# Kernel optimization log

Measured on AMD Instinct MI355X. Metric: run time of the kernel, lower is better.

The kernel has to match this reference:

```python
import jax, jax.numpy as jnp
import numpy as np

N, E, D = 100000, 1600000, 64
L = 3          # num_layers
EPS = 1e-5     # LayerNorm eps


def setup_inputs() -> dict:
    key = jax.random.key(0)
    ks = jax.random.split(key, 8)
    s = 0.05
    return {
        "x": jax.random.normal(ks[0], (N, D), jnp.float32),
        "edge_src": jax.random.randint(ks[1], (E,), 0, N, jnp.int32),
        "edge_dst": jax.random.randint(ks[2], (E,), 0, N, jnp.int32),
        # SAGEConv: lin_l (on aggregated neighbors, with bias), lin_r (root, no bias)
        "w_l": (jax.random.normal(ks[3], (L, D, D)) * s).astype(jnp.float32),
        "b_l": jnp.zeros((L, D), jnp.float32),
        "w_r": (jax.random.normal(ks[4], (L, D, D)) * s).astype(jnp.float32),
        # LayerNorm affine params per layer
        "gamma": jnp.ones((L, D), jnp.float32),
        "beta": jnp.zeros((L, D), jnp.float32),
        # residual projection (layer 0 only; Identity afterwards)
        "w_res": (jax.random.normal(ks[5], (D, D)) * s).astype(jnp.float32),
        "b_res": jnp.zeros((D,), jnp.float32),
        # final fc
        "w_fc": (jax.random.normal(ks[6], (D, D)) * s).astype(jnp.float32),
        "b_fc": jnp.zeros((D,), jnp.float32),
    }


def _layer_norm(h, g, b):
    mu = jnp.mean(h, axis=-1, keepdims=True)
    var = jnp.var(h, axis=-1, keepdims=True)
    return (h - mu) * jax.lax.rsqrt(var + EPS) * g + b


def reference(x, edge_src, edge_dst, w_l, b_l, w_r, gamma, beta, w_res, b_res, w_fc, b_fc):
    n = x.shape[0]
    # in-degree for mean aggregation (nodes with no in-edges get 0 aggregate)
    deg = jax.ops.segment_sum(jnp.ones(edge_dst.shape, x.dtype), edge_dst, num_segments=n)
    inv_deg = jnp.where(deg > 0, 1.0 / jnp.maximum(deg, 1.0), 0.0)[:, None]  # [N,1]
    for i in range(L):
        residual = x @ w_res + b_res if i == 0 else x
        # SAGEConv mean aggregation: gather source feats, scatter-sum at dst, divide by degree
        agg = jax.ops.segment_sum(x[edge_src], edge_dst, num_segments=n) * inv_deg  # [N,D]
        h = agg @ w_l[i] + b_l[i] + x @ w_r[i]
        h = jax.nn.relu(_layer_norm(h, gamma[i], beta[i]))
        # dropout is inactive in eval mode
        x = h + residual
    return x @ w_fc + b_fc
```

## Files before the change

### kernel.cpp

```cpp
#include <hip/hip_runtime.h>

typedef unsigned short u16;
typedef __bf16 bf16x8 __attribute__((ext_vector_type(8)));
typedef float f32x4 __attribute__((ext_vector_type(4)));

#define D 64
#define LPITCH 136
#define SPITCH 72
#define CHUNKS 512
#define BSHIFT 9

__device__ __forceinline__ float b2f(u16 u) {
    unsigned v = ((unsigned)u) << 16;
    float f;
    __builtin_memcpy(&f, &v, 4);
    return f;
}
__device__ __forceinline__ float u2f_lo(unsigned u) {
    unsigned v = u << 16;
    float f;
    __builtin_memcpy(&f, &v, 4);
    return f;
}
__device__ __forceinline__ float u2f_hi(unsigned u) {
    unsigned v = u & 0xFFFF0000u;
    float f;
    __builtin_memcpy(&f, &v, 4);
    return f;
}
__device__ __forceinline__ u16 f2b(float f) {
    unsigned u;
    __builtin_memcpy(&u, &f, 4);
    u = u + 0x7FFFu + ((u >> 16) & 1u);
    return (u16)(u >> 16);
}
__device__ __forceinline__ bf16x8 ld_frag(const u16* p) {
    union { uint4 u; bf16x8 b; } cv;
    cv.u = *(const uint4*)p;
    return cv.b;
}

__global__ __launch_bounds__(256) void binA_kernel(const int* __restrict__ dst, int E,
                                                   int* __restrict__ H,
                                                   int nbuck, int eper) {
    __shared__ int hist[256];
    int t = threadIdx.x;
    int c = blockIdx.x;
    hist[t] = 0;
    __syncthreads();
    int beg = c * eper;
    int end = min(beg + eper, E);
    for (int i = beg + t; i < end; i += 256) {
        atomicAdd(&hist[dst[i] >> BSHIFT], 1);
    }
    __syncthreads();
    if (t < nbuck) H[c * nbuck + t] = hist[t];
}

__global__ __launch_bounds__(256) void binS2_kernel(const int* __restrict__ H,
                                                    int* __restrict__ Orel,
                                                    int* __restrict__ T,
                                                    int nbuck) {
    __shared__ int ss[256];
    int b = blockIdx.x;
    int t = threadIdx.x;
    int h0 = H[(2 * t) * nbuck + b];
    int h1 = H[(2 * t + 1) * nbuck + b];
    ss[t] = h0 + h1;
    __syncthreads();
    for (int off = 1; off < 256; off <<= 1) {
        int v = (t >= off) ? ss[t - off] : 0;
        __syncthreads();
        ss[t] += v;
        __syncthreads();
    }
    int excl = ss[t] - h0 - h1;
    Orel[(2 * t) * nbuck + b] = excl;
    Orel[(2 * t + 1) * nbuck + b] = excl + h0;
    if (t == 255) T[b] = ss[255];
}

__global__ __launch_bounds__(256) void binT_kernel(const int* __restrict__ T, int nbuck,
                                                   int* __restrict__ base,
                                                   int* __restrict__ row_ptr, int N) {
    __shared__ int sm[256];
    int t = threadIdx.x;
    int v = (t < nbuck) ? T[t] : 0;
    sm[t] = v;
    __syncthreads();
    for (int off = 1; off < 256; off <<= 1) {
        int u = (t >= off) ? sm[t - off] : 0;
        __syncthreads();
        sm[t] += u;
        __syncthreads();
    }
    if (t < nbuck) base[t] = sm[t] - v;
    if (t == 255) {
        base[nbuck] = sm[255];
        row_ptr[N] = sm[255];
    }
}

__global__ __launch_bounds__(256) void binB_kernel(const int* __restrict__ src,
                                                   const int* __restrict__ dst, int E,
                                                   const int* __restrict__ base,
                                                   const int* __restrict__ Orel,
                                                   int* __restrict__ staging,
                                                   int nbuck, int eper) {
    __shared__ int pos[256];
    int t = threadIdx.x;
    int c = blockIdx.x;
    if (t < nbuck) pos[t] = base[t] + Orel[c * nbuck + t];
    __syncthreads();
    int beg = c * eper;
    int end = min(beg + eper, E);
    const int mask = (1 << BSHIFT) - 1;
    for (int i = beg + t; i < end; i += 256) {
        int d = dst[i];
        int b = d >> BSHIFT;
        int p = atomicAdd(&pos[b], 1);
        staging[p] = src[i] | ((d & mask) << 17);
    }
}

__global__ __launch_bounds__(256) void binC_kernel(const int* __restrict__ staging,
                                                   const int* __restrict__ base,
                                                   int* __restrict__ row_ptr,
                                                   float* __restrict__ inv_deg,
                                                   int* __restrict__ col, int N) {
    __shared__ int cnt[512];
    __shared__ int lrp[512];
    __shared__ int sm[256];
    int b = blockIdx.x;
    int t = threadIdx.x;
    int node0 = b << BSHIFT;
    int nn = min(1 << BSHIFT, N - node0);
    cnt[t] = 0;
    cnt[t + 256] = 0;
    __syncthreads();
    int sbeg = base[b], send = base[b + 1];
    for (int i = sbeg + t; i < send; i += 256) {
        atomicAdd(&cnt[staging[i] >> 17], 1);
    }
    __syncthreads();
    int c0 = cnt[2 * t], c1 = cnt[2 * t + 1];
    sm[t] = c0 + c1;
    __syncthreads();
    for (int off = 1; off < 256; off <<= 1) {
        int v = (t >= off) ? sm[t - off] : 0;
        __syncthreads();
        sm[t] += v;
        __syncthreads();
    }
    int excl = sm[t] - c0 - c1;
    lrp[2 * t] = excl;
    lrp[2 * t + 1] = excl + c0;
    __syncthreads();
    for (int i = t; i < nn; i += 256) {
        row_ptr[node0 + i] = sbeg + lrp[i];
        int dd = cnt[i];
        inv_deg[node0 + i] = dd > 0 ? 1.0f / (float)dd : 0.0f;
    }
    __syncthreads();
    for (int i = sbeg + t; i < send; i += 256) {
        int word = staging[i];
        int ld = word >> 17;
        int k = atomicSub(&cnt[ld], 1) - 1;
        col[sbeg + lrp[ld] + k] = word & 0x1FFFF;
    }
}

__global__ __launch_bounds__(256) void prep_w(const float* __restrict__ wl,
                                              const float* __restrict__ wr,
                                              const float* __restrict__ wres,
                                              const float* __restrict__ wfc,
                                              u16* __restrict__ WtL,
                                              u16* __restrict__ WresT,
                                              u16* __restrict__ WfcT) {
    int gid = blockIdx.x * 256 + threadIdx.x;
    int gstr = gridDim.x * 256;
    for (int idx = gid; idx < 3 * 64 * 128; idx += gstr) {
        int l = idx >> 13;
        int rem = idx & 8191;
        int n = rem >> 7;
        int k = rem & 127;
        float v = (k < 64) ? wl[l * 4096 + k * 64 + n] : wr[l * 4096 + (k - 64) * 64 + n];
        WtL[idx] = f2b(v);
    }
    for (int idx = gid; idx < 4096; idx += gstr) {
        int n = idx >> 6, k = idx & 63;
        WresT[idx] = f2b(wres[k * 64 + n]);
        WfcT[idx] = f2b(wfc[k * 64 + n]);
    }
}

__global__ __launch_bounds__(256) void cvt_kernel(const float* __restrict__ xf,
                                                  u16* __restrict__ xb, int total4) {
    int i = blockIdx.x * 256 + threadIdx.x;
    int stride = gridDim.x * 256;
    for (; i < total4; i += stride) {
        float4 v = *(const float4*)(xf + i * 4);
        ushort4 o;
        o.x = f2b(v.x); o.y = f2b(v.y); o.z = f2b(v.z); o.w = f2b(v.w);
        *(ushort4*)(xb + i * 4) = o;
    }
}

__global__ __launch_bounds__(256, 4) void layer_kernel(const u16* __restrict__ xb_in,
                                                       const int* __restrict__ row_ptr,
                                                       const int* __restrict__ col,
                                                       const float* __restrict__ inv_deg,
                                                       const u16* __restrict__ Wt,
                                                       const float* __restrict__ bl,
                                                       const float* __restrict__ gam,
                                                       const float* __restrict__ bet,
                                                       const u16* __restrict__ WresT,
                                                       const float* __restrict__ bres,
                                                       u16* __restrict__ xb_out,
                                                       int N, int layer0) {
    __shared__ __align__(16) u16 sA[64 * LPITCH];
    __shared__ __align__(16) u16 sB[64 * LPITCH];
    int tid = threadIdx.x;
    int base = blockIdx.x * 64;
    int lane = tid & 63;
    int w = tid >> 6;

#pragma unroll
    for (int i = 0; i < 4; i++) {
        int idx = i * 256 + tid;
        int r = idx >> 4, c = idx & 15;
        *(uint4*)&sB[r * LPITCH + c * 8] = *(const uint4*)(Wt + idx * 8);
    }
#pragma unroll
    for (int i = 0; i < 2; i++) {
        int idx = i * 256 + tid;
        int r = idx >> 3, c = idx & 7;
        int node = base + r;
        uint4 v = make_uint4(0, 0, 0, 0);
        if (node < N) v = *(const uint4*)(xb_in + node * D + c * 8);
        *(uint4*)&sA[r * LPITCH + 64 + c * 8] = v;
    }

    int slot = lane >> 3;
    int chunk = lane & 7;
#pragma unroll
    for (int r = 0; r < 2; r++) {
        int node_l = w * 16 + r * 8 + slot;
        int node = base + node_l;
        float a0 = 0, a1 = 0, a2 = 0, a3 = 0, a4 = 0, a5 = 0, a6 = 0, a7 = 0;
        uint4 o = make_uint4(0, 0, 0, 0);
        if (node < N) {
            int e = row_ptr[node], end = row_ptr[node + 1];
#define ACC(v)                                          \
    a0 += u2f_lo(v.x); a1 += u2f_hi(v.x);               \
    a2 += u2f_lo(v.y); a3 += u2f_hi(v.y);               \
    a4 += u2f_lo(v.z); a5 += u2f_hi(v.z);               \
    a6 += u2f_lo(v.w); a7 += u2f_hi(v.w);
            for (; e + 3 < end; e += 4) {
                int s0 = col[e], s1 = col[e + 1], s2 = col[e + 2], s3 = col[e + 3];
                uint4 v0 = *(const uint4*)(xb_in + s0 * D + chunk * 8);
                uint4 v1 = *(const uint4*)(xb_in + s1 * D + chunk * 8);
                uint4 v2 = *(const uint4*)(xb_in + s2 * D + chunk * 8);
                uint4 v3 = *(const uint4*)(xb_in + s3 * D + chunk * 8);
                ACC(v0) ACC(v1) ACC(v2) ACC(v3)
            }
            if (e + 1 < end) {
                int s0 = col[e], s1 = col[e + 1];
                uint4 v0 = *(const uint4*)(xb_in + s0 * D + chunk * 8);
                uint4 v1 = *(const uint4*)(xb_in + s1 * D + chunk * 8);
                ACC(v0) ACC(v1)
                e += 2;
            }
            if (e < end) {
                int s0 = col[e];
                uint4 v0 = *(const uint4*)(xb_in + s0 * D + chunk * 8);
                ACC(v0)
            }
#undef ACC
            float m = inv_deg[node];
            o.x = (unsigned)f2b(a0 * m) | ((unsigned)f2b(a1 * m) << 16);
            o.y = (unsigned)f2b(a2 * m) | ((unsigned)f2b(a3 * m) << 16);
            o.z = (unsigned)f2b(a4 * m) | ((unsigned)f2b(a5 * m) << 16);
            o.w = (unsigned)f2b(a6 * m) | ((unsigned)f2b(a7 * m) << 16);
        }
        *(uint4*)&sA[node_l * LPITCH + chunk * 8] = o;
    }
    __syncthreads();

    int q = lane >> 4;
    int ln = lane & 15;
    f32x4 acc[4] = {{0, 0, 0, 0}, {0, 0, 0, 0}, {0, 0, 0, 0}, {0, 0, 0, 0}};
    f32x4 accr[4] = {{0, 0, 0, 0}, {0, 0, 0, 0}, {0, 0, 0, 0}, {0, 0, 0, 0}};
    const u16* aRow = &sA[(w * 16 + ln) * LPITCH];

#pragma unroll
    for (int c = 0; c < 4; c++) {
        bf16x8 a = ld_frag(&aRow[c * 32 + q * 8]);
#pragma unroll
        for (int t = 0; t < 4; t++) {
            bf16x8 b = ld_frag(&sB[(t * 16 + ln) * LPITCH + c * 32 + q * 8]);
            acc[t] = __builtin_amdgcn_mfma_f32_16x16x32_bf16(a, b, acc[t], 0, 0, 0);
        }
    }
    if (layer0) {
#pragma unroll
        for (int c = 0; c < 2; c++) {
            bf16x8 a = ld_frag(&aRow[64 + c * 32 + q * 8]);
#pragma unroll
            for (int t = 0; t < 4; t++) {
                bf16x8 b = ld_frag(WresT + (t * 16 + ln) * 64 + c * 32 + q * 8);
                accr[t] = __builtin_amdgcn_mfma_f32_16x16x32_bf16(a, b, accr[t], 0, 0, 0);
            }
        }
    }

    float bcol[4], gcol[4], btcol[4], brcol[4];
#pragma unroll
    for (int t = 0; t < 4; t++) {
        int colI = t * 16 + ln;
        bcol[t] = bl[colI];
        gcol[t] = gam[colI];
        btcol[t] = bet[colI];
        brcol[t] = layer0 ? bres[colI] : 0.f;
    }
#pragma unroll
    for (int t = 0; t < 4; t++)
#pragma unroll
        for (int r = 0; r < 4; r++) acc[t][r] += bcol[t];

    float ps[4], pq[4];
#pragma unroll
    for (int r = 0; r < 4; r++) {
        float s = 0, s2 = 0;
#pragma unroll
        for (int t = 0; t < 4; t++) { float h = acc[t][r]; s += h; s2 += h * h; }
        ps[r] = s; pq[r] = s2;
    }
    for (int off = 1; off < 16; off <<= 1) {
#pragma unroll
        for (int r = 0; r < 4; r++) {
            ps[r] += __shfl_xor(ps[r], off, 64);
            pq[r] += __shfl_xor(pq[r], off, 64);
        }
    }
#pragma unroll
    for (int r = 0; r < 4; r++) {
        int nb = w * 16 + q * 4 + r;
        int node = base + nb;
        if (node >= N) continue;
        float mu = ps[r] * (1.f / 64.f);
        float var = pq[r] * (1.f / 64.f) - mu * mu;
        var = var < 0.f ? 0.f : var;
        float rstd = rsqrtf(var + 1e-5f);
#pragma unroll
        for (int t = 0; t < 4; t++) {
            int colI = t * 16 + ln;
            float hn = (acc[t][r] - mu) * rstd * gcol[t] + btcol[t];
            hn = hn > 0.f ? hn : 0.f;
            float res = layer0 ? (accr[t][r] + brcol[t])
                               : b2f(sA[nb * LPITCH + 64 + colI]);
            xb_out[node * D + colI] = f2b(hn + res);
        }
    }
}

__global__ __launch_bounds__(256) void fc_kernel(const u16* __restrict__ xbin,
                                                 const u16* __restrict__ WfcT,
                                                 const float* __restrict__ bfc,
                                                 float* __restrict__ out, int N) {
    __shared__ __align__(16) u16 sA[64 * SPITCH];
    __shared__ __align__(16) u16 sB[64 * SPITCH];
    int tid = threadIdx.x;
    int base = blockIdx.x * 64;
#pragma unroll
    for (int i = 0; i < 2; i++) {
        int idx = i * 256 + tid;
        int r = idx >> 3, c = idx & 7;
        int node = base + r;
        uint4 v = make_uint4(0, 0, 0, 0);
        if (node < N) v = *(const uint4*)(xbin + node * D + c * 8);
        *(uint4*)&sA[r * SPITCH + c * 8] = v;
        *(uint4*)&sB[r * SPITCH + c * 8] = *(const uint4*)(WfcT + idx * 8);
    }
    __syncthreads();
    int lane = tid & 63;
    int w = tid >> 6, q = lane >> 4, ln = lane & 15;
    f32x4 acc[4] = {{0, 0, 0, 0}, {0, 0, 0, 0}, {0, 0, 0, 0}, {0, 0, 0, 0}};
#pragma unroll
    for (int c = 0; c < 2; c++) {
        bf16x8 a = ld_frag(&sA[(w * 16 + ln) * SPITCH + c * 32 + q * 8]);
#pragma unroll
        for (int t = 0; t < 4; t++) {
            bf16x8 b = ld_frag(&sB[(t * 16 + ln) * SPITCH + c * 32 + q * 8]);
            acc[t] = __builtin_amdgcn_mfma_f32_16x16x32_bf16(a, b, acc[t], 0, 0, 0);
        }
    }
#pragma unroll
    for (int r = 0; r < 4; r++) {
        int node = base + w * 16 + q * 4 + r;
        if (node >= N) continue;
#pragma unroll
        for (int t = 0; t < 4; t++) {
            int colI = t * 16 + ln;
            out[node * D + colI] = acc[t][r] + bfc[colI];
        }
    }
}

extern "C" void kernel_launch(void* const* d_in, const int* in_sizes, int n_in,
                              void* d_out, int out_size, void* d_ws, size_t ws_size,
                              hipStream_t stream) {
    const float* x_in = (const float*)d_in[0];
    const int* e_src = (const int*)d_in[1];
    const int* e_dst = (const int*)d_in[2];
    const float* w_l = (const float*)d_in[3];
    const float* b_l = (const float*)d_in[4];
    const float* w_r = (const float*)d_in[5];
    const float* gam = (const float*)d_in[6];
    const float* bet = (const float*)d_in[7];
    const float* w_res = (const float*)d_in[8];
    const float* b_res = (const float*)d_in[9];
    const float* w_fc = (const float*)d_in[10];
    const float* b_fc = (const float*)d_in[11];
    float* out = (float*)d_out;

    const int N = in_sizes[0] / D;
    const int E = in_sizes[1];
    const int nbuck = ((N - 1) >> BSHIFT) + 1;
    const int eper = (E + CHUNKS - 1) / CHUNKS;

    size_t o = 0;
    auto carve = [&](size_t bytes) {
        size_t cur = o;
        o += (bytes + 255) & ~(size_t)255;
        return (char*)d_ws + cur;
    };
    int* row_ptr = (int*)carve((size_t)(N + 1) * 4);
    float* inv_deg = (float*)carve((size_t)N * 4);
    int* colA = (int*)carve((size_t)E * 4);
    int* staging = (int*)carve((size_t)E * 4);
    int* Hh = (int*)carve((size_t)CHUNKS * nbuck * 4);
    int* Orel = (int*)carve((size_t)CHUNKS * nbuck * 4);
    int* Tb = (int*)carve((size_t)nbuck * 4);
    int* baseB = (int*)carve((size_t)(nbuck + 1) * 4);
    u16* WtL = (u16*)carve(3 * 64 * 128 * 2);
    u16* WresT = (u16*)carve(64 * 64 * 2);
    u16* WfcT = (u16*)carve(64 * 64 * 2);
    u16* xbA = (u16*)carve((size_t)N * D * 2);
    u16* xbB = (u16*)carve((size_t)N * D * 2);

    binA_kernel<<<CHUNKS, 256, 0, stream>>>(e_dst, E, Hh, nbuck, eper);
    binS2_kernel<<<nbuck, 256, 0, stream>>>(Hh, Orel, Tb, nbuck);
    binT_kernel<<<1, 256, 0, stream>>>(Tb, nbuck, baseB, row_ptr, N);
    binB_kernel<<<CHUNKS, 256, 0, stream>>>(e_src, e_dst, E, baseB, Orel, staging, nbuck, eper);
    binC_kernel<<<nbuck, 256, 0, stream>>>(staging, baseB, row_ptr, inv_deg, colA, N);

    prep_w<<<32, 256, 0, stream>>>(w_l, w_r, w_res, w_fc, WtL, WresT, WfcT);
    cvt_kernel<<<1024, 256, 0, stream>>>(x_in, xbA, N * D / 4);

    int gridT = (N + 63) / 64;

    layer_kernel<<<gridT, 256, 0, stream>>>(xbA, row_ptr, colA, inv_deg, WtL,
                                            b_l, gam, bet, WresT, b_res, xbB, N, 1);
    layer_kernel<<<gridT, 256, 0, stream>>>(xbB, row_ptr, colA, inv_deg, WtL + 8192,
                                            b_l + 64, gam + 64, bet + 64, WresT, b_res,
                                            xbA, N, 0);
    layer_kernel<<<gridT, 256, 0, stream>>>(xbA, row_ptr, colA, inv_deg, WtL + 16384,
                                            b_l + 128, gam + 128, bet + 128, WresT, b_res,
                                            xbB, N, 0);
    fc_kernel<<<gridT, 256, 0, stream>>>(xbB, WfcT, b_fc, out, N);
}
```

Measured before the change: 289.9 us.

## Fuse final FC into last layer, drop weight LDS staging, halve binning chunks

Folds the final fully-connected projection into the third layer kernel, which writes its bf16 result back into LDS and runs the FC MFMA in place. This removes one launch and a full round trip of the activations through global memory. Layer weights are now read as MFMA fragments straight from global/L2 instead of being staged into a second LDS buffer, which frees LDS so the occupancy hint can rise from 4 to 6 blocks. The binning histogram uses 256 chunks with a simpler one-entry-per-thread scan. The extra final_ branch and the global weight fragment loads may cost some latency in exchange.

Result: slower. 330.0 us (+13.8%).

```diff
diff --git a/kernel.cpp b/kernel.cpp
--- a/kernel.cpp
+++ b/kernel.cpp
@@ -7,7 +7,7 @@
 #define D 64
 #define LPITCH 136
 #define SPITCH 72
-#define CHUNKS 512
+#define CHUNKS 256
 #define BSHIFT 9
 
 __device__ __forceinline__ float b2f(u16 u) {
@@ -64,9 +64,8 @@
     __shared__ int ss[256];
     int b = blockIdx.x;
     int t = threadIdx.x;
-    int h0 = H[(2 * t) * nbuck + b];
-    int h1 = H[(2 * t + 1) * nbuck + b];
-    ss[t] = h0 + h1;
+    int h = H[t * nbuck + b];
+    ss[t] = h;
     __syncthreads();
     for (int off = 1; off < 256; off <<= 1) {
         int v = (t >= off) ? ss[t - off] : 0;
@@ -74,9 +73,7 @@
         ss[t] += v;
         __syncthreads();
     }
-    int excl = ss[t] - h0 - h1;
-    Orel[(2 * t) * nbuck + b] = excl;
-    Orel[(2 * t + 1) * nbuck + b] = excl + h0;
+    Orel[t * nbuck + b] = ss[t] - h;
     if (t == 255) T[b] = ss[255];
 }
 
@@ -206,7 +203,7 @@
     }
 }
 
-__global__ __launch_bounds__(256, 4) void layer_kernel(const u16* __restrict__ xb_in,
+__global__ __launch_bounds__(256, 6) void layer_kernel(const u16* __restrict__ xb_in,
                                                        const int* __restrict__ row_ptr,
                                                        const int* __restrict__ col,
                                                        const float* __restrict__ inv_deg,
@@ -216,21 +213,17 @@
                                                        const float* __restrict__ bet,
                                                        const u16* __restrict__ WresT,
                                                        const float* __restrict__ bres,
+                                                       const u16* __restrict__ WfcT,
+                                                       const float* __restrict__ bfc,
                                                        u16* __restrict__ xb_out,
-                                                       int N, int layer0) {
+                                                       float* __restrict__ fout,
+                                                       int N, int layer0, int final_) {
     __shared__ __align__(16) u16 sA[64 * LPITCH];
-    __shared__ __align__(16) u16 sB[64 * LPITCH];
     int tid = threadIdx.x;
     int base = blockIdx.x * 64;
     int lane = tid & 63;
     int w = tid >> 6;
 
-#pragma unroll
-    for (int i = 0; i < 4; i++) {
-        int idx = i * 256 + tid;
-        int r = idx >> 4, c = idx & 15;
-        *(uint4*)&sB[r * LPITCH + c * 8] = *(const uint4*)(Wt + idx * 8);
-    }
 #pragma unroll
     for (int i = 0; i < 2; i++) {
         int idx = i * 256 + tid;
@@ -298,7 +291,7 @@
         bf16x8 a = ld_frag(&aRow[c * 32 + q * 8]);
 #pragma unroll
         for (int t = 0; t < 4; t++) {
-            bf16x8 b = ld_frag(&sB[(t * 16 + ln) * LPITCH + c * 32 + q * 8]);
+            bf16x8 b = ld_frag(Wt + (t * 16 + ln) * 128 + c * 32 + q * 8);
             acc[t] = __builtin_amdgcn_mfma_f32_16x16x32_bf16(a, b, acc[t], 0, 0, 0);
         }
     }
@@ -359,50 +352,32 @@
             hn = hn > 0.f ? hn : 0.f;
             float res = layer0 ? (accr[t][r] + brcol[t])
                                : b2f(sA[nb * LPITCH + 64 + colI]);
-            xb_out[node * D + colI] = f2b(hn + res);
-        }
-    }
-}
-
-__global__ __launch_bounds__(256) void fc_kernel(const u16* __restrict__ xbin,
-                                                 const u16* __restrict__ WfcT,
-                                                 const float* __restrict__ bfc,
-                                                 float* __restrict__ out, int N) {
-    __shared__ __align__(16) u16 sA[64 * SPITCH];
-    __shared__ __align__(16) u16 sB[64 * SPITCH];
-    int tid = threadIdx.x;
-    int base = blockIdx.x * 64;
-#pragma unroll
-    for (int i = 0; i < 2; i++) {
-        int idx = i * 256 + tid;
-        int r = idx >> 3, c = idx & 7;
-        int node = base + r;
-        uint4 v = make_uint4(0, 0, 0, 0);
-        if (node < N) v = *(const uint4*)(xbin + node * D + c * 8);
-        *(uint4*)&sA[r * SPITCH + c * 8] = v;
-        *(uint4*)&sB[r * SPITCH + c * 8] = *(const uint4*)(WfcT + idx * 8);
-    }
-    __syncthreads();
-    int lane = tid & 63;
-    int w = tid >> 6, q = lane >> 4, ln = lane & 15;
-    f32x4 acc[4] = {{0, 0, 0, 0}, {0, 0, 0, 0}, {0, 0, 0, 0}, {0, 0, 0, 0}};
-#pragma unroll
-    for (int c = 0; c < 2; c++) {
-        bf16x8 a = ld_frag(&sA[(w * 16 + ln) * SPITCH + c * 32 + q * 8]);
-#pragma unroll
-        for (int t = 0; t < 4; t++) {
-            bf16x8 b = ld_frag(&sB[(t * 16 + ln) * SPITCH + c * 32 + q * 8]);
-            acc[t] = __builtin_amdgcn_mfma_f32_16x16x32_bf16(a, b, acc[t], 0, 0, 0);
-        }
-    }
-#pragma unroll
-    for (int r = 0; r < 4; r++) {
-        int node = base + w * 16 + q * 4 + r;
-        if (node >= N) continue;
-#pragma unroll
-        for (int t = 0; t < 4; t++) {
-            int colI = t * 16 + ln;
-            out[node * D + colI] = acc[t][r] + bfc[colI];
+            u16 vb = f2b(hn + res);
+            if (final_) sA[nb * LPITCH + colI] = vb;
+            else xb_out[node * D + colI] = vb;
+        }
+    }
+
+    if (final_) {
+        f32x4 accf[4] = {{0, 0, 0, 0}, {0, 0, 0, 0}, {0, 0, 0, 0}, {0, 0, 0, 0}};
+#pragma unroll
+        for (int c = 0; c < 2; c++) {
+            bf16x8 a = ld_frag(&aRow[c * 32 + q * 8]);
+#pragma unroll
+            for (int t = 0; t < 4; t++) {
+                bf16x8 b = ld_frag(WfcT + (t * 16 + ln) * 64 + c * 32 + q * 8);
+                accf[t] = __builtin_amdgcn_mfma_f32_16x16x32_bf16(a, b, accf[t], 0, 0, 0);
+            }
+        }
+#pragma unroll
+        for (int r = 0; r < 4; r++) {
+            int node = base + w * 16 + q * 4 + r;
+            if (node >= N) continue;
+#pragma unroll
+            for (int t = 0; t < 4; t++) {
+                int colI = t * 16 + ln;
+                fout[node * D + colI] = accf[t][r] + bfc[colI];
+            }
         }
     }
 }
@@ -461,12 +436,12 @@
     int gridT = (N + 63) / 64;
 
     layer_kernel<<<gridT, 256, 0, stream>>>(xbA, row_ptr, colA, inv_deg, WtL,
-                                            b_l, gam, bet, WresT, b_res, xbB, N, 1);
+                                            b_l, gam, bet, WresT, b_res,
+                                            WfcT, b_fc, xbB, out, N, 1, 0);
     layer_kernel<<<gridT, 256, 0, stream>>>(xbB, row_ptr, colA, inv_deg, WtL + 8192,
                                             b_l + 64, gam + 64, bet + 64, WresT, b_res,
-                                            xbA, N, 0);
+                                            WfcT, b_fc, xbA, out, N, 0, 0);
     layer_kernel<<<gridT, 256, 0, stream>>>(xbA, row_ptr, colA, inv_deg, WtL + 16384,
                                             b_l + 128, gam + 128, bet + 128, WresT, b_res,
-                                            xbB, N, 0);
-    fc_kernel<<<gridT, 256, 0, stream>>>(xbB, WfcT, b_fc, out, N);
-}
+                                            WfcT, b_fc, xbB, out, N, 0, 1);
+}
```
